# Optimization experiments

Measured on AMD Instinct MI355X. Metric: run time of the kernel, lower is better.

## Reference

```python
import jax, jax.numpy as jnp
import numpy as np

D = 512

def _resmlp(x, W1, W2):
    # residual MLP: x + silu(x W1) W2  (e3nn-style bias-free linears)
    return x + jax.nn.silu(x @ W1) @ W2

def setup_inputs() -> dict:
    key = jax.random.key(0)
    ks = jax.random.split(key, 12)
    s = 1.0 / np.sqrt(D)
    mk = lambda k: jax.random.normal(k, (D, D), dtype=jnp.float32) * s
    return {
        "x": jax.random.normal(ks[0], (4, 4096, D), dtype=jnp.float32),
        "qW1": mk(ks[1]), "qW2": mk(ks[2]),
        "kW1": mk(ks[3]), "kW2": mk(ks[4]),
        "vW1": mk(ks[5]), "vW2": mk(ks[6]),
        "aWq": mk(ks[7]), "aWk": mk(ks[8]), "aWv": mk(ks[9]),
        "Wout": mk(ks[10]),
    }

def reference(x, qW1, qW2, kW1, kW2, vW1, vW2, aWq, aWk, aWv, Wout):
    # ResiMLP q/k/v projections on node features [B, N, D]
    q = _resmlp(x, qW1, qW2) @ aWq
    k = _resmlp(x, kW1, kW2) @ aWk
    v = _resmlp(x, vW1, vW2) @ aWv
    # naive full attention: bmm -> softmax(dim=1, over QUERY axis) -> bmm
    attn = jnp.einsum("bqd,bkd->bqk", q, k)   # [B, Nq, Nk]
    attn = jax.nn.softmax(attn, axis=1)        # faithful to Softmax(dim=1)
    out = jnp.einsum("bqk,bkd->bqd", attn, v)  # [B, N, D]
    return out @ Wout
```

## Files before the change

kernel.cpp:

```cpp
#include <hip/hip_runtime.h>
#include <hip/hip_bf16.h>
#include <stdint.h>
#include <stddef.h>

typedef _Float16 f16;
typedef __attribute__((ext_vector_type(8))) _Float16 f16x8;
typedef __attribute__((ext_vector_type(4))) float f32x4;

#define EPI_NONE 0
#define EPI_SILU 1
#define EPI_RES  2
#define OUT_F16    0
#define OUT_F32    1
#define OUT_VT     3
#define OUT_ESTATS 4
#define OUT_QKV    5

__device__ __forceinline__ void gll16(const f16* g, char* l) {
    __builtin_amdgcn_global_load_lds(
        (const __attribute__((address_space(1))) void*)g,
        (__attribute__((address_space(3))) void*)l, 16, 0, 0);
}

template<int BN, int EPI, int OUT, int AEC, int SWZ2D>
__global__ __launch_bounds__(256)
void gemm_f16(const f16* __restrict__ A, const f16* __restrict__ Bm,
              void* __restrict__ Cp, f16* __restrict__ Cp2,
              const float* __restrict__ Res,
              float* __restrict__ mp, float* __restrict__ zp,
              const float* __restrict__ cScale,
              int kseg, int lda, int ldb, int ldc, int ldr,
              unsigned long long sA, unsigned long long sB, unsigned long long sC)
{
    constexpr int NWF = BN / 32;
    constexpr int NCH = BN / 8;
    constexpr int LCH = (BN == 128) ? 4 : 3;

    const size_t zC = (size_t)blockIdx.z * sC;

    unsigned bxs, bys;
    if constexpr (SWZ2D) {
        unsigned lin = blockIdx.y * 32 + blockIdx.x;
        unsigned c = lin & 7, idx = lin >> 3;
        bys = (c >> 2) * 16 + (idx >> 3);
        bxs = (c & 3) * 8 + (idx & 7);
    } else {
        unsigned nwg = gridDim.x * gridDim.y;
        unsigned lin = blockIdx.y * gridDim.x + blockIdx.x;
        unsigned cpx = nwg >> 3;
        unsigned swz = (lin & 7) * cpx + (lin >> 3);
        bxs = swz % gridDim.x; bys = swz / gridDim.x;
    }

    const int t    = threadIdx.x;
    const int w    = t >> 6;
    const int lane = t & 63;
    const int wr   = w >> 1, wc = w & 1;
    const int lo   = lane & 15, hi = lane >> 4;
    const int brow = bys * 128;
    const int bcol = bxs * BN;

    const f16* Ag = A + (size_t)blockIdx.z * sA;
    const f16* Bg = Bm + (size_t)blockIdx.z * sB;
    if constexpr (OUT == OUT_QKV) Ag += (size_t)(bcol >> 9) * 512;

    __shared__ __align__(16) char ldsbuf[16384 + BN * 128];
    f16* As = (f16*)ldsbuf;
    f16* Bs = (f16*)(ldsbuf + 16384);
    float* smst = (float*)ldsbuf;
    f16* Ls = (f16*)ldsbuf;

    f32x4 acc[4][NWF];
#pragma unroll
    for (int m = 0; m < 4; ++m)
#pragma unroll
        for (int n = 0; n < NWF; ++n)
            acc[m][n] = (f32x4){0.f, 0.f, 0.f, 0.f};

    const int r0 = t >> 3;
    const int cswz = ((t & 7) ^ ((t >> 3) & 7)) * 8;
    const int rA7  = lo & 7;

    const float* cb = nullptr;
    f16x8 bq[NWF];
    float4 cq0, cq1;
    if constexpr (AEC) {
        cb = cScale + ((size_t)blockIdx.z * 32 + (brow >> 7)) * 4096;
#pragma unroll
        for (int i = 0; i < NWF; ++i)
            bq[i] = *(const f16x8*)(Bg + (size_t)(bcol + i * 32 + r0) * ldb + cswz);
        cq0 = *(const float4*)(cb + cswz);
        cq1 = *(const float4*)(cb + cswz + 4);
    }

    for (int k0 = 0; k0 < kseg; k0 += 64) {
#pragma unroll
        for (int i = 0; i < 4; ++i)
            gll16(Ag + (size_t)(brow + i * 32 + r0) * lda + (k0 + cswz),
                  (char*)As + i * 4096 + w * 1024);
        if constexpr (AEC) {
            float cf[8] = {cq0.x, cq0.y, cq0.z, cq0.w, cq1.x, cq1.y, cq1.z, cq1.w};
#pragma unroll
            for (int i = 0; i < NWF; ++i) {
                f16x8 ev = bq[i], pv;
#pragma unroll
                for (int j = 0; j < 8; ++j) pv[j] = (f16)((float)ev[j] * cf[j]);
                *(f16x8*)((char*)Bs + i * 4096 + t * 16) = pv;
            }
            if (k0 + 64 < kseg) {
#pragma unroll
                for (int i = 0; i < NWF; ++i)
                    bq[i] = *(const f16x8*)(Bg + (size_t)(bcol + i * 32 + r0) * ldb
                                            + (k0 + 64 + cswz));
                cq0 = *(const float4*)(cb + k0 + 64 + cswz);
                cq1 = *(const float4*)(cb + k0 + 64 + cswz + 4);
            }
        } else {
#pragma unroll
            for (int i = 0; i < NWF; ++i)
                gll16(Bg + (size_t)(bcol + i * 32 + r0) * ldb + (k0 + cswz),
                      (char*)Bs + i * 4096 + w * 1024);
        }
        __syncthreads();

#pragma unroll
        for (int kk = 0; kk < 64; kk += 32) {
            f16x8 aH[4], bH[NWF];
#pragma unroll
            for (int m = 0; m < 4; ++m) {
                int idx = (wr * 64 + m * 16 + lo) * 64 +
                          ((((kk >> 3) + hi) ^ rA7) * 8);
                aH[m] = *(const f16x8*)&As[idx];
            }
#pragma unroll
            for (int n = 0; n < NWF; ++n) {
                int idx = (wc * (BN / 2) + n * 16 + lo) * 64 +
                          ((((kk >> 3) + hi) ^ rA7) * 8);
                bH[n] = *(const f16x8*)&Bs[idx];
            }
#pragma unroll
            for (int m = 0; m < 4; ++m)
#pragma unroll
                for (int n = 0; n < NWF; ++n)
                    acc[m][n] = __builtin_amdgcn_mfma_f32_16x16x32_f16(
                        aH[m], bH[n], acc[m][n], 0, 0, 0);
        }
        __syncthreads();
    }

    if constexpr (OUT == OUT_ESTATS) {
        const size_t zS = (size_t)blockIdx.z * (32 * 4096);
        float mb[NWF];
#pragma unroll
        for (int n = 0; n < NWF; ++n) {
            float ml = acc[0][n][0];
#pragma unroll
            for (int m = 0; m < 4; ++m)
#pragma unroll
                for (int j = 0; j < 4; ++j) ml = fmaxf(ml, acc[m][n][j]);
            ml = fmaxf(ml, __shfl_xor(ml, 16));
            ml = fmaxf(ml, __shfl_xor(ml, 32));
            if (hi == 0) smst[wr * 128 + wc * 64 + n * 16 + lo] = ml;
        }
        __syncthreads();
#pragma unroll
        for (int n = 0; n < NWF; ++n) {
            int c = wc * 64 + n * 16 + lo;
            mb[n] = fmaxf(smst[c], smst[128 + c]);
        }
        __syncthreads();
        float zsum[NWF];
#pragma unroll
        for (int n = 0; n < NWF; ++n) {
            zsum[n] = 0.f;
            int lcol = wc * 64 + n * 16 + lo;
#pragma unroll
            for (int m = 0; m < 4; ++m)
#pragma unroll
                for (int j = 0; j < 4; ++j) {
                    int lrow = wr * 64 + m * 16 + hi * 4 + j;
                    float e = __expf(acc[m][n][j] - mb[n]);
                    zsum[n] += e;
                    Ls[lrow * BN + lcol] = (f16)e;
                }
        }
        __syncthreads();
        for (int i = t; i < 128 * NCH; i += 256) {
            int r2 = i >> LCH, cc = i & (NCH - 1);
            f16x8 vv = *(const f16x8*)&Ls[r2 * BN + cc * 8];
            *(f16x8*)&((f16*)Cp)[(size_t)(brow + r2) * ldc + bcol + cc * 8 + zC] = vv;
        }
        __syncthreads();
#pragma unroll
        for (int n = 0; n < NWF; ++n) {
            float zl = zsum[n];
            zl += __shfl_xor(zl, 16);
            zl += __shfl_xor(zl, 32);
            if (hi == 0) smst[wr * 128 + wc * 64 + n * 16 + lo] = zl;
        }
        __syncthreads();
        size_t o = zS + (size_t)(brow >> 7) * 4096 + bcol;
        if (t < 128) zp[o + t] = smst[t] + smst[128 + t];
        if (wr == 0 && hi == 0) {
#pragma unroll
            for (int n = 0; n < NWF; ++n)
                mp[o + wc * 64 + n * 16 + lo] = mb[n];
        }
        return;
    }

    if constexpr (OUT == OUT_F16 || OUT == OUT_QKV) {
        bool packed = (OUT == OUT_F16) || (bcol < 1024);
        if (packed) {
#pragma unroll
            for (int m = 0; m < 4; ++m)
#pragma unroll
                for (int n = 0; n < NWF; ++n)
#pragma unroll
                    for (int j = 0; j < 4; ++j) {
                        int lrow = wr * 64 + m * 16 + hi * 4 + j;
                        int lcol = wc * (BN / 2) + n * 16 + lo;
                        float v = acc[m][n][j];
                        if (EPI == EPI_SILU) v = v / (1.f + __expf(-v));
                        if (EPI == EPI_RES)
                            v += Res[(size_t)(brow + lrow) * ldr + bcol + lcol];
                        Ls[lrow * BN + lcol] = (f16)v;
                    }
            __syncthreads();
            for (int i = t; i < 128 * NCH; i += 256) {
                int r2 = i >> LCH, cc = i & (NCH - 1);
                f16x8 vv = *(const f16x8*)&Ls[r2 * BN + cc * 8];
                *(f16x8*)&((f16*)Cp)[(size_t)(brow + r2) * ldc + bcol + cc * 8 + zC] = vv;
            }
        } else {
#pragma unroll
            for (int m = 0; m < 4; ++m)
#pragma unroll
                for (int n = 0; n < NWF; ++n) {
                    int row0 = brow + wr * 64 + m * 16 + hi * 4;
                    int col  = bcol + wc * (BN / 2) + n * 16 + lo - 1024;
                    int bb = row0 >> 12, n0 = row0 & 4095;
                    unsigned short u[4];
#pragma unroll
                    for (int j = 0; j < 4; ++j) {
                        f16 vb = (f16)acc[m][n][j];
                        u[j] = *(unsigned short*)&vb;
                    }
                    ushort4 pack = {u[0], u[1], u[2], u[3]};
                    *(ushort4*)&Cp2[((size_t)(bb * 512 + col) << 12) + n0] = pack;
                }
        }
        return;
    }

#pragma unroll
    for (int m = 0; m < 4; ++m) {
#pragma unroll
        for (int n = 0; n < NWF; ++n) {
            if constexpr (OUT == OUT_VT) {
                int row0 = brow + wr * 64 + m * 16 + hi * 4;
                int col  = bcol + wc * (BN / 2) + n * 16 + lo;
                int bb = row0 >> 12, n0 = row0 & 4095;
                unsigned short u[4];
#pragma unroll
                for (int j = 0; j < 4; ++j) {
                    f16 vb = (f16)acc[m][n][j];
                    u[j] = *(unsigned short*)&vb;
                }
                ushort4 pack = {u[0], u[1], u[2], u[3]};
                *(ushort4*)&((f16*)Cp)[((size_t)(bb * 512 + col) << 12) + n0] = pack;
            } else {
#pragma unroll
                for (int j = 0; j < 4; ++j) {
                    int row = brow + wr * 64 + m * 16 + hi * 4 + j;
                    int col = bcol + wc * (BN / 2) + n * 16 + lo;
                    size_t idx = (size_t)row * ldc + col + zC;
                    float v = acc[m][n][j];
                    if (EPI == EPI_SILU) v = v / (1.f + __expf(-v));
                    if (EPI == EPI_RES)  v += Res[(size_t)row * ldr + col];
                    ((float*)Cp)[idx] = v;
                }
            }
        }
    }
}

__global__ void cast_x_kernel(const float* __restrict__ x, f16* __restrict__ xf)
{
    size_t i = ((size_t)blockIdx.x * 256 + threadIdx.x) * 8;
    float4 a = *(const float4*)(x + i);
    float4 b = *(const float4*)(x + i + 4);
    f16x8 o;
    o[0] = (f16)a.x; o[1] = (f16)a.y; o[2] = (f16)a.z; o[3] = (f16)a.w;
    o[4] = (f16)b.x; o[5] = (f16)b.y; o[6] = (f16)b.z; o[7] = (f16)b.w;
    *(f16x8*)(xf + i) = o;
}

struct WPack { const float* W[10]; f16* H[10]; };

__global__ void transw_all_kernel(WPack p)
{
    const float* W = p.W[blockIdx.z];
    f16* WT = p.H[blockIdx.z];
    __shared__ float tile[32][33];
    int bx = blockIdx.x * 32, by = blockIdx.y * 32;
    int tx = threadIdx.x, ty = threadIdx.y;
#pragma unroll
    for (int i = 0; i < 32; i += 8)
        tile[ty + i][tx] = W[(size_t)(by + ty + i) * 512 + bx + tx];
    __syncthreads();
#pragma unroll
    for (int i = 0; i < 32; i += 8)
        WT[(size_t)(bx + ty + i) * 512 + by + tx] = (f16)tile[tx][ty + i];
}

__global__ void colstats_comb_kernel(const float* __restrict__ mp,
                                     const float* __restrict__ zp,
                                     float* __restrict__ cB)
{
    size_t base = (size_t)blockIdx.y * (32 * 4096);
    int col = blockIdx.x * 256 + threadIdx.x;
    float m = -1e30f;
#pragma unroll
    for (int i = 0; i < 32; ++i) m = fmaxf(m, mp[base + i * 4096 + col]);
    float z = 0.f;
#pragma unroll
    for (int i = 0; i < 32; ++i)
        z += zp[base + i * 4096 + col] * __expf(mp[base + i * 4096 + col] - m);
    float r = 1.f / z;
#pragma unroll
    for (int i = 0; i < 32; ++i)
        cB[base + i * 4096 + col] = __expf(mp[base + i * 4096 + col] - m) * r;
}

extern "C" void kernel_launch(void* const* d_in, const int* in_sizes, int n_in,
                              void* d_out, int out_size, void* d_ws, size_t ws_size,
                              hipStream_t stream)
{
    const int B = 4, N = 4096, D = 512;
    const size_t MALL = (size_t)B * N;
    const size_t ND = MALL * D;
    const size_t NN = (size_t)N * N;
    const size_t WW = (size_t)D * D;
    const float* x = (const float*)d_in[0];
    const float* Wf[10];
    for (int i = 0; i < 10; ++i) Wf[i] = (const float*)d_in[1 + i];

    char* ws = (char*)d_ws;
    size_t off = 0;
    auto carve = [&](size_t bytes) -> char* {
        char* p = ws + off;
        off = (off + bytes + 255) & ~(size_t)255;
        return p;
    };

    const size_t PLANE = NN * 2;
    f16* E_all = (f16*)carve(4 * PLANE);
    f16* QKf   = (f16*)carve(PLANE);
    f16* VT    = (f16*)carve((size_t)B * D * N * 2);
    f16* O     = (f16*)carve(ND * 2);
    f16* wc1   = (f16*)carve(3 * WW * 2);
    f16* wc2   = (f16*)carve(3 * WW * 2);
    f16* wcA   = (f16*)carve(3 * WW * 2);
    f16* wo    = (f16*)carve(WW * 2);
    float* mp  = (float*)carve((size_t)B * 32 * 4096 * 4);
    float* zp  = (float*)carve((size_t)B * 32 * 4096 * 4);
    float* cB  = (float*)carve((size_t)B * 32 * 4096 * 4);

    f16* xf = E_all;
    f16* t1 = E_all + ND;
    f16* h  = t1 + MALL * 1536;
    (void)in_sizes; (void)n_in; (void)out_size; (void)ws_size;

    cast_x_kernel<<<dim3((unsigned)(ND / 2048)), 256, 0, stream>>>(x, xf);
    WPack wp;
    wp.W[0] = Wf[0]; wp.H[0] = wc1;
    wp.W[1] = Wf[2]; wp.H[1] = wc1 + WW;
    wp.W[2] = Wf[4]; wp.H[2] = wc1 + 2 * WW;
    wp.W[3] = Wf[1]; wp.H[3] = wc2;
    wp.W[4] = Wf[3]; wp.H[4] = wc2 + WW;
    wp.W[5] = Wf[5]; wp.H[5] = wc2 + 2 * WW;
    wp.W[6] = Wf[6]; wp.H[6] = wcA;
    wp.W[7] = Wf[7]; wp.H[7] = wcA + WW;
    wp.W[8] = Wf[8]; wp.H[8] = wcA + 2 * WW;
    wp.W[9] = Wf[9]; wp.H[9] = wo;
    transw_all_kernel<<<dim3(16, 16, 10), dim3(32, 8), 0, stream>>>(wp);

    gemm_f16<128, EPI_SILU, OUT_F16, 0, 0><<<dim3(12, 128), 256, 0, stream>>>(
        xf, wc1, t1, nullptr, nullptr, nullptr, nullptr, nullptr,
        512, 512, 512, 1536, 512, 0, 0, 0);
    gemm_f16<128, EPI_RES, OUT_F16, 0, 0><<<dim3(4, 128, 3), 256, 0, stream>>>(
        t1, wc2, h, nullptr, x, nullptr, nullptr, nullptr,
        512, 1536, 512, 1536, 512, 512, WW, 512);
    gemm_f16<128, EPI_NONE, OUT_QKV, 0, 0><<<dim3(12, 128), 256, 0, stream>>>(
        h, wcA, QKf, VT, nullptr, nullptr, nullptr, nullptr,
        512, 1536, 512, 1024, 512, 0, 0, 0);

    gemm_f16<128, EPI_NONE, OUT_ESTATS, 0, 1><<<dim3(32, 32, 4), 256, 0, stream>>>(
        QKf, QKf + 512, E_all, nullptr, nullptr, mp, zp, nullptr,
        512, 1024, 1024, 4096, 4096,
        (unsigned long long)N * 1024, (unsigned long long)N * 1024, NN);
    colstats_comb_kernel<<<dim3(16, 4), 256, 0, stream>>>(mp, zp, cB);

    gemm_f16<64, EPI_NONE, OUT_F16, 1, 0><<<dim3(8, 32, 4), 256, 0, stream>>>(
        E_all, VT, O, nullptr, nullptr, nullptr, nullptr, cB,
        4096, 4096, 4096, 512, 512,
        NN, (unsigned long long)D * N, (unsigned long long)N * D);

    gemm_f16<128, EPI_NONE, OUT_F32, 0, 0><<<dim3(4, 128), 256, 0, stream>>>(
        O, wo, d_out, nullptr, nullptr, nullptr, nullptr, nullptr,
        512, 512, 512, 512, 512, 0, 0, 0);
}
```

Baseline: 363.0 us.

## Split-K the attention-V GEMM into two halves and sum them in the output projection

The E·V GEMM grid is doubled along z, and each block covers half of the key dimension (2048), writing its partial result to one of two halves of O. The final Wout GEMM adds the two partial halves while staging A into LDS, replacing the global_load_lds path for that GEMM. This is meant to fix the low occupancy of the 256-block E·V launch. It also XOR-swizzles the LDS epilogue staging to avoid bank conflicts and reads the residual from the fp16 x copy instead of the fp32 x. The residual now carries fp16 rounding, and the partial sums are rounded to fp16 before being added.

Result: no change. 367.9 us (+1.4%).

```diff
diff --git a/kernel.cpp b/kernel.cpp
--- a/kernel.cpp
+++ b/kernel.cpp
@@ -22,11 +22,11 @@
         (__attribute__((address_space(3))) void*)l, 16, 0, 0);
 }
 
-template<int BN, int EPI, int OUT, int AEC, int SWZ2D>
+template<int BN, int EPI, int OUT, int AEC, int SWZ2D, int DECZ, int ASUM>
 __global__ __launch_bounds__(256)
 void gemm_f16(const f16* __restrict__ A, const f16* __restrict__ Bm,
               void* __restrict__ Cp, f16* __restrict__ Cp2,
-              const float* __restrict__ Res,
+              const f16* __restrict__ Res,
               float* __restrict__ mp, float* __restrict__ zp,
               const float* __restrict__ cScale,
               int kseg, int lda, int ldb, int ldc, int ldr,
@@ -35,8 +35,11 @@
     constexpr int NWF = BN / 32;
     constexpr int NCH = BN / 8;
     constexpr int LCH = (BN == 128) ? 4 : 3;
-
-    const size_t zC = (size_t)blockIdx.z * sC;
+    const size_t OHALF = 8388608;
+
+    int zb = blockIdx.z, kh = 0;
+    if constexpr (DECZ) { kh = zb >> 2; zb &= 3; }
+    const size_t zC = (size_t)zb * sC + (size_t)kh * OHALF;
 
     unsigned bxs, bys;
     if constexpr (SWZ2D) {
@@ -60,8 +63,8 @@
     const int brow = bys * 128;
     const int bcol = bxs * BN;
 
-    const f16* Ag = A + (size_t)blockIdx.z * sA;
-    const f16* Bg = Bm + (size_t)blockIdx.z * sB;
+    const f16* Ag = A + (size_t)zb * sA + kh * 2048;
+    const f16* Bg = Bm + (size_t)zb * sB + kh * 2048;
     if constexpr (OUT == OUT_QKV) Ag += (size_t)(bcol >> 9) * 512;
 
     __shared__ __align__(16) char ldsbuf[16384 + BN * 128];
@@ -69,6 +72,7 @@
     f16* Bs = (f16*)(ldsbuf + 16384);
     float* smst = (float*)ldsbuf;
     f16* Ls = (f16*)ldsbuf;
+    auto lsX = [](int r, int c) { return (c ^ (((r >> 2) & 3) << 4)); };
 
     f32x4 acc[4][NWF];
 #pragma unroll
@@ -85,19 +89,44 @@
     f16x8 bq[NWF];
     float4 cq0, cq1;
     if constexpr (AEC) {
-        cb = cScale + ((size_t)blockIdx.z * 32 + (brow >> 7)) * 4096;
+        cb = cScale + ((size_t)zb * 32 + (brow >> 7)) * 4096 + kh * 2048;
 #pragma unroll
         for (int i = 0; i < NWF; ++i)
             bq[i] = *(const f16x8*)(Bg + (size_t)(bcol + i * 32 + r0) * ldb + cswz);
         cq0 = *(const float4*)(cb + cswz);
         cq1 = *(const float4*)(cb + cswz + 4);
     }
+    f16x8 aq0[4], aq1[4];
+    if constexpr (ASUM) {
+#pragma unroll
+        for (int i = 0; i < 4; ++i) {
+            size_t off = (size_t)(brow + i * 32 + r0) * lda + cswz;
+            aq0[i] = *(const f16x8*)(Ag + off);
+            aq1[i] = *(const f16x8*)(Ag + off + OHALF);
+        }
+    }
 
     for (int k0 = 0; k0 < kseg; k0 += 64) {
-#pragma unroll
-        for (int i = 0; i < 4; ++i)
-            gll16(Ag + (size_t)(brow + i * 32 + r0) * lda + (k0 + cswz),
-                  (char*)As + i * 4096 + w * 1024);
+        if constexpr (ASUM) {
+#pragma unroll
+            for (int i = 0; i < 4; ++i) {
+                f16x8 s = aq0[i] + aq1[i];
+                *(f16x8*)((char*)As + i * 4096 + t * 16) = s;
+            }
+            if (k0 + 64 < kseg) {
+#pragma unroll
+                for (int i = 0; i < 4; ++i) {
+                    size_t off = (size_t)(brow + i * 32 + r0) * lda + k0 + 64 + cswz;
+                    aq0[i] = *(const f16x8*)(Ag + off);
+                    aq1[i] = *(const f16x8*)(Ag + off + OHALF);
+                }
+            }
+        } else {
+#pragma unroll
+            for (int i = 0; i < 4; ++i)
+                gll16(Ag + (size_t)(brow + i * 32 + r0) * lda + (k0 + cswz),
+                      (char*)As + i * 4096 + w * 1024);
+        }
         if constexpr (AEC) {
             float cf[8] = {cq0.x, cq0.y, cq0.z, cq0.w, cq1.x, cq1.y, cq1.z, cq1.w};
 #pragma unroll
@@ -149,7 +178,7 @@
     }
 
     if constexpr (OUT == OUT_ESTATS) {
-        const size_t zS = (size_t)blockIdx.z * (32 * 4096);
+        const size_t zS = (size_t)zb * (32 * 4096);
         float mb[NWF];
 #pragma unroll
         for (int n = 0; n < NWF; ++n) {
@@ -181,13 +210,13 @@
                     int lrow = wr * 64 + m * 16 + hi * 4 + j;
                     float e = __expf(acc[m][n][j] - mb[n]);
                     zsum[n] += e;
-                    Ls[lrow * BN + lcol] = (f16)e;
+                    Ls[lrow * BN + lsX(lrow, lcol)] = (f16)e;
                 }
         }
         __syncthreads();
         for (int i = t; i < 128 * NCH; i += 256) {
             int r2 = i >> LCH, cc = i & (NCH - 1);
-            f16x8 vv = *(const f16x8*)&Ls[r2 * BN + cc * 8];
+            f16x8 vv = *(const f16x8*)&Ls[r2 * BN + lsX(r2, cc * 8)];
             *(f16x8*)&((f16*)Cp)[(size_t)(brow + r2) * ldc + bcol + cc * 8 + zC] = vv;
         }
         __syncthreads();
@@ -223,13 +252,13 @@
                         float v = acc[m][n][j];
                         if (EPI == EPI_SILU) v = v / (1.f + __expf(-v));
                         if (EPI == EPI_RES)
-                            v += Res[(size_t)(brow + lrow) * ldr + bcol + lcol];
-                        Ls[lrow * BN + lcol] = (f16)v;
+                            v += (float)Res[(size_t)(brow + lrow) * ldr + bcol + lcol];
+                        Ls[lrow * BN + lsX(lrow, lcol)] = (f16)v;
                     }
             __syncthreads();
             for (int i = t; i < 128 * NCH; i += 256) {
                 int r2 = i >> LCH, cc = i & (NCH - 1);
-                f16x8 vv = *(const f16x8*)&Ls[r2 * BN + cc * 8];
+                f16x8 vv = *(const f16x8*)&Ls[r2 * BN + lsX(r2, cc * 8)];
                 *(f16x8*)&((f16*)Cp)[(size_t)(brow + r2) * ldc + bcol + cc * 8 + zC] = vv;
             }
         } else {
@@ -277,7 +306,7 @@
                     size_t idx = (size_t)row * ldc + col + zC;
                     float v = acc[m][n][j];
                     if (EPI == EPI_SILU) v = v / (1.f + __expf(-v));
-                    if (EPI == EPI_RES)  v += Res[(size_t)row * ldr + col];
+                    if (EPI == EPI_RES)  v += (float)Res[(size_t)row * ldr + col];
                     ((float*)Cp)[idx] = v;
                 }
             }
@@ -358,7 +387,7 @@
     f16* E_all = (f16*)carve(4 * PLANE);
     f16* QKf   = (f16*)carve(PLANE);
     f16* VT    = (f16*)carve((size_t)B * D * N * 2);
-    f16* O     = (f16*)carve(ND * 2);
+    f16* O     = (f16*)carve(2 * ND * 2);
     f16* wc1   = (f16*)carve(3 * WW * 2);
     f16* wc2   = (f16*)carve(3 * WW * 2);
     f16* wcA   = (f16*)carve(3 * WW * 2);
@@ -386,28 +415,28 @@
     wp.W[9] = Wf[9]; wp.H[9] = wo;
     transw_all_kernel<<<dim3(16, 16, 10), dim3(32, 8), 0, stream>>>(wp);
 
-    gemm_f16<128, EPI_SILU, OUT_F16, 0, 0><<<dim3(12, 128), 256, 0, stream>>>(
+    gemm_f16<128, EPI_SILU, OUT_F16, 0, 0, 0, 0><<<dim3(12, 128), 256, 0, stream>>>(
         xf, wc1, t1, nullptr, nullptr, nullptr, nullptr, nullptr,
         512, 512, 512, 1536, 512, 0, 0, 0);
-    gemm_f16<128, EPI_RES, OUT_F16, 0, 0><<<dim3(4, 128, 3), 256, 0, stream>>>(
-        t1, wc2, h, nullptr, x, nullptr, nullptr, nullptr,
+    gemm_f16<128, EPI_RES, OUT_F16, 0, 0, 0, 0><<<dim3(4, 128, 3), 256, 0, stream>>>(
+        t1, wc2, h, nullptr, xf, nullptr, nullptr, nullptr,
         512, 1536, 512, 1536, 512, 512, WW, 512);
-    gemm_f16<128, EPI_NONE, OUT_QKV, 0, 0><<<dim3(12, 128), 256, 0, stream>>>(
+    gemm_f16<128, EPI_NONE, OUT_QKV, 0, 0, 0, 0><<<dim3(12, 128), 256, 0, stream>>>(
         h, wcA, QKf, VT, nullptr, nullptr, nullptr, nullptr,
         512, 1536, 512, 1024, 512, 0, 0, 0);
 
-    gemm_f16<128, EPI_NONE, OUT_ESTATS, 0, 1><<<dim3(32, 32, 4), 256, 0, stream>>>(
+    gemm_f16<128, EPI_NONE, OUT_ESTATS, 0, 1, 0, 0><<<dim3(32, 32, 4), 256, 0, stream>>>(
         QKf, QKf + 512, E_all, nullptr, nullptr, mp, zp, nullptr,
         512, 1024, 1024, 4096, 4096,
         (unsigned long long)N * 1024, (unsigned long long)N * 1024, NN);
     colstats_comb_kernel<<<dim3(16, 4), 256, 0, stream>>>(mp, zp, cB);
 
-    gemm_f16<64, EPI_NONE, OUT_F16, 1, 0><<<dim3(8, 32, 4), 256, 0, stream>>>(
+    gemm_f16<64, EPI_NONE, OUT_F16, 1, 0, 1, 0><<<dim3(8, 32, 8), 256, 0, stream>>>(
         E_all, VT, O, nullptr, nullptr, nullptr, nullptr, cB,
-        4096, 4096, 4096, 512, 512,
+        2048, 4096, 4096, 512, 512,
         NN, (unsigned long long)D * N, (unsigned long long)N * D);
 
-    gemm_f16<128, EPI_NONE, OUT_F32, 0, 0><<<dim3(4, 128), 256, 0, stream>>>(
+    gemm_f16<128, EPI_NONE, OUT_F32, 0, 0, 0, 1><<<dim3(4, 128), 256, 0, stream>>>(
         O, wo, d_out, nullptr, nullptr, nullptr, nullptr, nullptr,
         512, 512, 512, 512, 512, 0, 0, 0);
 }
```
